# Optimization experiments

Measured on AMD Instinct MI355X. Metric: run time of the kernel, lower is better.

## Reference

```python
import jax, jax.numpy as jnp
import numpy as np

EPSILON = 0.1
NUM_ITERS = 50
D = 256


def setup_inputs() -> dict:
    key = jax.random.key(0)
    ks = jax.random.split(key, 12)
    NA, NT = 8192, 8192
    s = 1.0 / np.sqrt(D)
    return {
        "agent_embeddings": jax.random.normal(ks[0], (NA, D), jnp.float32),
        "task_embeddings": jax.random.normal(ks[1], (NT, D), jnp.float32),
        "Wq": jax.random.normal(ks[2], (D, D), jnp.float32) * s,
        "bq": jax.random.normal(ks[3], (D,), jnp.float32) * 0.01,
        "Wk": jax.random.normal(ks[4], (D, D), jnp.float32) * s,
        "bk": jax.random.normal(ks[5], (D,), jnp.float32) * 0.01,
        "W1": jax.random.normal(ks[6], (D, D // 2), jnp.float32) * s,
        "b1": jax.random.normal(ks[7], (D // 2,), jnp.float32) * 0.01,
        "W2": jax.random.normal(ks[8], (D // 2, 1), jnp.float32) * (1.0 / np.sqrt(D // 2)),
        "b2": jax.random.normal(ks[9], (1,), jnp.float32) * 0.01,
    }


def _ot_forward(agent_embeddings, task_embeddings, Wq, bq, Wk, bk, W1, b1, W2, b2):
    num_tasks = task_embeddings.shape[0]
    q = agent_embeddings @ Wq + bq  # [NA, D]
    k = task_embeddings @ Wk + bk   # [NT, D]
    q_norm = jnp.sum(q * q, axis=1, keepdims=True)          # [NA, 1]
    k_norm = jnp.sum(k * k, axis=1, keepdims=True)          # [NT, 1]
    distances = q_norm + k_norm.T - 2.0 * (q @ k.T)          # [NA, NT]
    C = -distances
    supply_logits = (jax.nn.relu(agent_embeddings @ W1 + b1) @ W2 + b2)[:, 0]
    b = jax.nn.softmax(supply_logits, axis=0)                # [NA]
    a = jnp.ones((num_tasks,), dtype=C.dtype) / num_tasks    # [NT]

    log_b = jnp.log(b + 1e-20)
    log_a = jnp.log(a + 1e-20)
    log_K = -C / EPSILON                                     # [NA, NT]

    def body(_, fg):
        f, g = fg
        f = log_b - jax.nn.logsumexp(log_K + g[None, :], axis=1)
        g = log_a - jax.nn.logsumexp(log_K + f[:, None], axis=0)
        return (f, g)

    f0 = jnp.zeros_like(b)
    g0 = jnp.zeros_like(a)
    f, g = jax.lax.fori_loop(0, NUM_ITERS, body, (f0, g0))

    T = jnp.exp(f[:, None] + log_K + g[None, :])
    T = jnp.maximum(T, 0.0)
    T = T / (jnp.sum(T) + 1e-08)
    return T


def reference(agent_embeddings, task_embeddings, Wq, bq, Wk, bk, W1, b1, W2, b2):
    return _ot_forward(agent_embeddings, task_embeddings, Wq, bq, Wk, bk, W1, b1, W2, b2)
```

## Files before the change

### kernel.cpp

```cpp
#include <hip/hip_runtime.h>
#include <math.h>

#define NR 8192
#define DIM 256
#define NBLK 512
#define CROWS 16
#define RSC 2
#define NSUB 8
#define SCALE2 14.426950408889634f

__device__ __forceinline__ float fexp2(float x) {
#if __has_builtin(__builtin_amdgcn_exp2f)
    return __builtin_amdgcn_exp2f(x);
#else
    return exp2f(x);
#endif
}
__device__ __forceinline__ float flog2(float x) {
#if __has_builtin(__builtin_amdgcn_logf)
    return __builtin_amdgcn_logf(x);
#else
    return log2f(x);
#endif
}

__device__ __forceinline__ void gl2lds16(const float* gp, float* lp) {
#if __has_builtin(__builtin_amdgcn_global_load_lds)
    __builtin_amdgcn_global_load_lds(
        (const __attribute__((address_space(1))) unsigned int*)gp,
        (__attribute__((address_space(3))) unsigned int*)lp, 16, 0, 0);
#else
    *(float4*)lp = *(const float4*)gp;
#endif
}

__device__ __forceinline__ void wait_vm0()  { asm volatile("s_waitcnt vmcnt(0)" ::: "memory"); }
__device__ __forceinline__ void bar_lgkm()  { asm volatile("s_waitcnt lgkmcnt(0)\ns_barrier" ::: "memory"); }

__device__ __forceinline__ void lse_comb2(float& m, float& s, float mo, float so) {
    float nm = fmaxf(m, mo);
    s = s * fexp2(m - nm) + so * fexp2(mo - nm);
    m = nm;
}

__device__ __forceinline__ void lse_upd4(float& m, float& s,
                                         float v0, float v1, float v2, float v3) {
    float m4 = fmaxf(fmaxf(v0, v1), fmaxf(v2, v3));
    float nm = fmaxf(m, m4);
    float e = fexp2(v0 - nm) + fexp2(v1 - nm) + fexp2(v2 - nm) + fexp2(v3 - nm);
    s = fmaf(s, fexp2(m - nm), e);
    m = nm;
}

__device__ __forceinline__ void lse_upd2(float& m, float& s, float v0, float v1) {
    float m2 = fmaxf(v0, v1);
    float nm = fmaxf(m, m2);
    float e = fexp2(v0 - nm) + fexp2(v1 - nm);
    s = fmaf(s, fexp2(m - nm), e);
    m = nm;
}

__global__ void init_zero(float* __restrict__ g) {
    int t = blockIdx.x * 256 + threadIdx.x;
    if (t < NR) g[t] = 0.0f;
}

__global__ __launch_bounds__(256) void gemm_qk(const float* __restrict__ A,
                                               const float* __restrict__ W,
                                               const float* __restrict__ bias,
                                               float* __restrict__ out) {
    __shared__ float As[16][68];
    __shared__ float Ws[16][68];
    const int t  = threadIdx.x;
    const int r0 = blockIdx.x * 64;
    const int c0 = blockIdx.y * 64;
    const int ty = t >> 4, tx = t & 15;
    const int arow = t >> 2;
    const int ak   = (t & 3) * 4;
    const int wrow = t >> 4;
    const int wcol = (t & 15) * 4;
    float acc[4][4] = {};
    for (int k0 = 0; k0 < DIM; k0 += 16) {
        float4 av = *(const float4*)(A + (size_t)(r0 + arow) * DIM + k0 + ak);
        float4 wv = *(const float4*)(W + (size_t)(k0 + wrow) * DIM + c0 + wcol);
        __syncthreads();
        As[ak + 0][arow] = av.x; As[ak + 1][arow] = av.y;
        As[ak + 2][arow] = av.z; As[ak + 3][arow] = av.w;
        *(float4*)&Ws[wrow][wcol] = wv;
        __syncthreads();
#pragma unroll
        for (int kk = 0; kk < 16; ++kk) {
            float4 a = *(const float4*)&As[kk][ty * 4];
            float4 b = *(const float4*)&Ws[kk][tx * 4];
            float aa[4] = {a.x, a.y, a.z, a.w};
            float bb[4] = {b.x, b.y, b.z, b.w};
#pragma unroll
            for (int i = 0; i < 4; ++i)
#pragma unroll
                for (int j = 0; j < 4; ++j)
                    acc[i][j] = fmaf(aa[i], bb[j], acc[i][j]);
        }
    }
#pragma unroll
    for (int i = 0; i < 4; ++i) {
        float4 o;
        o.x = acc[i][0] + bias[c0 + tx * 4 + 0];
        o.y = acc[i][1] + bias[c0 + tx * 4 + 1];
        o.z = acc[i][2] + bias[c0 + tx * 4 + 2];
        o.w = acc[i][3] + bias[c0 + tx * 4 + 3];
        *(float4*)(out + (size_t)(r0 + ty * 4 + i) * DIM + c0 + tx * 4) = o;
    }
}

__global__ __launch_bounds__(64) void row_norm(const float* __restrict__ x,
                                               float* __restrict__ out) {
    const int row = blockIdx.x, lane = threadIdx.x;
    float4 v = *(const float4*)(x + (size_t)row * DIM + lane * 4);
    float s = v.x * v.x + v.y * v.y + v.z * v.z + v.w * v.w;
#pragma unroll
    for (int off = 32; off > 0; off >>= 1) s += __shfl_xor(s, off);
    if (lane == 0) out[row] = s;
}

__global__ __launch_bounds__(128) void mlp_logits(const float* __restrict__ A,
                                                  const float* __restrict__ W1,
                                                  const float* __restrict__ b1,
                                                  const float* __restrict__ W2,
                                                  const float* __restrict__ b2,
                                                  float* __restrict__ logits) {
    __shared__ float ar[DIM];
    __shared__ float red[2];
    const int t = threadIdx.x;
    const int row = blockIdx.x;
    *(float2*)&ar[t * 2] = *(const float2*)(A + (size_t)row * DIM + t * 2);
    __syncthreads();
    float h = b1[t];
#pragma unroll 8
    for (int kk = 0; kk < DIM; ++kk) h = fmaf(ar[kk], W1[kk * 128 + t], h);
    float val = fmaxf(h, 0.0f) * W2[t];
#pragma unroll
    for (int off = 32; off > 0; off >>= 1) val += __shfl_xor(val, off);
    if ((t & 63) == 0) red[t >> 6] = val;
    __syncthreads();
    if (t == 0) logits[row] = red[0] + red[1] + b2[0];
}

__global__ __launch_bounds__(1024) void softmax_logb(const float* __restrict__ logits,
                                                     float* __restrict__ logb2) {
    __shared__ float redm[16], reds[16];
    const int t = threadIdx.x;
    float l[8];
    float m = -INFINITY;
#pragma unroll
    for (int i = 0; i < 8; ++i) { l[i] = logits[i * 1024 + t]; m = fmaxf(m, l[i]); }
#pragma unroll
    for (int off = 32; off > 0; off >>= 1) m = fmaxf(m, __shfl_xor(m, off));
    if ((t & 63) == 0) redm[t >> 6] = m;
    __syncthreads();
    if (t < 64) {
        float v = (t < 16) ? redm[t] : -INFINITY;
#pragma unroll
        for (int off = 8; off > 0; off >>= 1) v = fmaxf(v, __shfl_xor(v, off));
        if (t == 0) redm[0] = v;
    }
    __syncthreads();
    m = redm[0];
    float s = 0.0f;
#pragma unroll
    for (int i = 0; i < 8; ++i) s += __expf(l[i] - m);
#pragma unroll
    for (int off = 32; off > 0; off >>= 1) s += __shfl_xor(s, off);
    if ((t & 63) == 0) reds[t >> 6] = s;
    __syncthreads();
    if (t < 64) {
        float v = (t < 16) ? reds[t] : 0.0f;
#pragma unroll
        for (int off = 8; off > 0; off >>= 1) v += __shfl_xor(v, off);
        if (t == 0) reds[0] = v;
    }
    __syncthreads();
    s = reds[0];
    float invs = 1.0f / s;
#pragma unroll
    for (int i = 0; i < 8; ++i)
        logb2[i * 1024 + t] = log2f(__expf(l[i] - m) * invs + 1e-20f);
}

__global__ __launch_bounds__(256) void dist_kernel(const float* __restrict__ q,
                                                   const float* __restrict__ k,
                                                   const float* __restrict__ qn,
                                                   const float* __restrict__ kn,
                                                   float* __restrict__ S) {
    __shared__ float Qs[16][132];
    __shared__ float Ks[16][132];
    const int t  = threadIdx.x;
    const int r0 = blockIdx.y * 128;
    const int c0 = blockIdx.x * 128;
    const int lrow = t >> 1;
    const int lk   = (t & 1) * 8;
    const int wv   = t >> 6;
    const int lane = t & 63;
    const int ty8 = (wv >> 1) * 8 + (lane >> 3);
    const int tx8 = (wv & 1) * 8 + (lane & 7);
    float acc[8][8] = {};
    for (int k0 = 0; k0 < DIM; k0 += 16) {
        float4 qa = *(const float4*)(q + (size_t)(r0 + lrow) * DIM + k0 + lk);
        float4 qb = *(const float4*)(q + (size_t)(r0 + lrow) * DIM + k0 + lk + 4);
        float4 ka = *(const float4*)(k + (size_t)(c0 + lrow) * DIM + k0 + lk);
        float4 kb = *(const float4*)(k + (size_t)(c0 + lrow) * DIM + k0 + lk + 4);
        __syncthreads();
        Qs[lk + 0][lrow] = qa.x; Qs[lk + 1][lrow] = qa.y;
        Qs[lk + 2][lrow] = qa.z; Qs[lk + 3][lrow] = qa.w;
        Qs[lk + 4][lrow] = qb.x; Qs[lk + 5][lrow] = qb.y;
        Qs[lk + 6][lrow] = qb.z; Qs[lk + 7][lrow] = qb.w;
        Ks[lk + 0][lrow] = ka.x; Ks[lk + 1][lrow] = ka.y;
        Ks[lk + 2][lrow] = ka.z; Ks[lk + 3][lrow] = ka.w;
        Ks[lk + 4][lrow] = kb.x; Ks[lk + 5][lrow] = kb.y;
        Ks[lk + 6][lrow] = kb.z; Ks[lk + 7][lrow] = kb.w;
        __syncthreads();
#pragma unroll
        for (int kk = 0; kk < 16; ++kk) {
            float4 a0 = *(const float4*)&Qs[kk][ty8 * 8];
            float4 a1 = *(const float4*)&Qs[kk][ty8 * 8 + 4];
            float4 b0 = *(const float4*)&Ks[kk][tx8 * 8];
            float4 b1 = *(const float4*)&Ks[kk][tx8 * 8 + 4];
            float aa[8] = {a0.x, a0.y, a0.z, a0.w, a1.x, a1.y, a1.z, a1.w};
            float bb[8] = {b0.x, b0.y, b0.z, b0.w, b1.x, b1.y, b1.z, b1.w};
#pragma unroll
            for (int i = 0; i < 8; ++i)
#pragma unroll
                for (int j = 0; j < 8; ++j)
                    acc[i][j] = fmaf(aa[i], bb[j], acc[i][j]);
        }
    }
    float knv[8];
#pragma unroll
    for (int j = 0; j < 8; ++j) knv[j] = kn[c0 + tx8 * 8 + j];
#pragma unroll
    for (int i = 0; i < 8; ++i) {
        const int row = r0 + ty8 * 8 + i;
        const float qni = qn[row];
        float* outp = S + (size_t)row * NR + c0 + tx8 * 8;
        float4 o0, o1;
        o0.x = (qni + knv[0] - 2.0f * acc[i][0]) * SCALE2;
        o0.y = (qni + knv[1] - 2.0f * acc[i][1]) * SCALE2;
        o0.z = (qni + knv[2] - 2.0f * acc[i][2]) * SCALE2;
        o0.w = (qni + knv[3] - 2.0f * acc[i][3]) * SCALE2;
        o1.x = (qni + knv[4] - 2.0f * acc[i][4]) * SCALE2;
        o1.y = (qni + knv[5] - 2.0f * acc[i][5]) * SCALE2;
        o1.z = (qni + knv[6] - 2.0f * acc[i][6]) * SCALE2;
        o1.w = (qni + knv[7] - 2.0f * acc[i][7]) * SCALE2;
        *(float4*)outp = o0;
        *(float4*)(outp + 4) = o1;
    }
}

__global__ __launch_bounds__(512, 4) void iter_fused(const float* __restrict__ S,
                                                     const float* __restrict__ g,
                                                     const float* __restrict__ logb2,
                                                     float* __restrict__ f,
                                                     float* __restrict__ pm) {
    __shared__ float buf[RSC][NR];
    __shared__ float redm[8], reds[8];
    const int t = threadIdx.x;
    const int wv = t >> 6, lane = t & 63;
    const int chunk = blockIdx.x;
    const int r0 = chunk * CROWS;
    const int rw = wv >> 2;
    const int qt = wv & 3;
    const int qbase = qt * 2048;
    const int loff = lane * 4;

    float4 greg[8];
#pragma unroll
    for (int it = 0; it < 8; ++it)
        greg[it] = *(const float4*)(g + qbase + it * 256 + loff);

    float cm[4][4], cs[4][4];
#pragma unroll
    for (int j = 0; j < 4; ++j)
#pragma unroll
        for (int c = 0; c < 4; ++c) { cm[j][c] = -INFINITY; cs[j][c] = 0.0f; }

    {
        const float* Sr = S + (size_t)(r0 + rw) * NR + qbase;
        float* ld = &buf[rw][qbase];
#pragma unroll
        for (int it = 0; it < 8; ++it)
#if __has_builtin(__builtin_amdgcn_global_load_lds)
            gl2lds16(Sr + it * 256 + loff, ld + it * 256);
#else
            gl2lds16(Sr + it * 256 + loff, ld + it * 256 + loff);
#endif
    }

    for (int sc = 0; sc < NSUB; ++sc) {
        wait_vm0();
        float m = -INFINITY, s = 0.0f;
#pragma unroll
        for (int it = 0; it < 8; ++it) {
            float4 v = *(const float4*)&buf[rw][qbase + it * 256 + loff];
            float4 gv = greg[it];
            lse_upd4(m, s, v.x + gv.x, v.y + gv.y, v.z + gv.z, v.w + gv.w);
        }
#pragma unroll
        for (int off = 32; off > 0; off >>= 1) {
            float mo = __shfl_xor(m, off);
            float so = __shfl_xor(s, off);
            lse_comb2(m, s, mo, so);
        }
        if (lane == 0) { redm[wv] = m; reds[wv] = s; }
        bar_lgkm();

        float fr[RSC];
#pragma unroll
        for (int r = 0; r < RSC; ++r) {
            float mm = redm[r * 4 + 0], ss = reds[r * 4 + 0];
            lse_comb2(mm, ss, redm[r * 4 + 1], reds[r * 4 + 1]);
            lse_comb2(mm, ss, redm[r * 4 + 2], reds[r * 4 + 2]);
            lse_comb2(mm, ss, redm[r * 4 + 3], reds[r * 4 + 3]);
            fr[r] = logb2[r0 + sc * RSC + r] - (mm + flog2(ss));
        }
        if (t < RSC) f[r0 + sc * RSC + t] = fr[t];

#pragma unroll
        for (int j = 0; j < 4; ++j) {
            const int c = j * 2048 + t * 4;
            float4 a = *(const float4*)&buf[0][c];
            float4 bb = *(const float4*)&buf[1][c];
            lse_upd2(cm[j][0], cs[j][0], a.x + fr[0], bb.x + fr[1]);
            lse_upd2(cm[j][1], cs[j][1], a.y + fr[0], bb.y + fr[1]);
            lse_upd2(cm[j][2], cs[j][2], a.z + fr[0], bb.z + fr[1]);
            lse_upd2(cm[j][3], cs[j][3], a.w + fr[0], bb.w + fr[1]);
        }
        bar_lgkm();

        if (sc + 1 < NSUB) {
            const float* Sn = S + (size_t)(r0 + (sc + 1) * RSC + rw) * NR + qbase;
            float* ld = &buf[rw][qbase];
#pragma unroll
            for (int it = 0; it < 8; ++it)
#if __has_builtin(__builtin_amdgcn_global_load_lds)
                gl2lds16(Sn + it * 256 + loff, ld + it * 256);
#else
                gl2lds16(Sn + it * 256 + loff, ld + it * 256 + loff);
#endif
        }
    }
#pragma unroll
    for (int j = 0; j < 4; ++j) {
        float4 L;
        L.x = cm[j][0] + flog2(cs[j][0]);
        L.y = cm[j][1] + flog2(cs[j][1]);
        L.z = cm[j][2] + flog2(cs[j][2]);
        L.w = cm[j][3] + flog2(cs[j][3]);
        *(float4*)&pm[(size_t)chunk * NR + j * 2048 + t * 4] = L;
    }
}

__global__ __launch_bounds__(256) void col_combine(const float* __restrict__ pm,
                                                   float* __restrict__ g,
                                                   float log_a2) {
    __shared__ float Lsh[8][32];
    const int cl = threadIdx.x & 31;
    const int gp = threadIdx.x >> 5;
    const int col = blockIdx.x * 32 + cl;
    float m = -INFINITY, s = 0.0f;
#pragma unroll
    for (int ch = gp * 64; ch < gp * 64 + 64; ch += 4) {
        float l0 = pm[(size_t)(ch + 0) * NR + col];
        float l1 = pm[(size_t)(ch + 1) * NR + col];
        float l2 = pm[(size_t)(ch + 2) * NR + col];
        float l3 = pm[(size_t)(ch + 3) * NR + col];
        lse_upd4(m, s, l0, l1, l2, l3);
    }
    Lsh[gp][cl] = m + flog2(s);
    __syncthreads();
    if (gp == 0) {
        float mm = -INFINITY, ss = 0.0f;
        lse_upd4(mm, ss, Lsh[0][cl], Lsh[1][cl], Lsh[2][cl], Lsh[3][cl]);
        lse_upd4(mm, ss, Lsh[4][cl], Lsh[5][cl], Lsh[6][cl], Lsh[7][cl]);
        g[col] = log_a2 - (mm + flog2(ss));
    }
}

__global__ __launch_bounds__(256) void write_pass(const float* S,
                                                  const float* __restrict__ f,
                                                  const float* __restrict__ g,
                                                  float* out) {
    const int wv = threadIdx.x >> 6, lane = threadIdx.x & 63;
    const int row = blockIdx.x * 4 + wv;
    const float fi = f[row];
    const float4* Sr = (const float4*)(S + (size_t)row * NR);
    const float4* gr = (const float4*)g;
    float4* Or = (float4*)(out + (size_t)row * NR);
#pragma unroll 4
    for (int it = 0; it < NR / 256; ++it) {
        const int idx = it * 64 + lane;
        float4 sv = Sr[idx];
        float4 gv = gr[idx];
        float4 o;
        o.x = fexp2(fi + sv.x + gv.x);
        o.y = fexp2(fi + sv.y + gv.y);
        o.z = fexp2(fi + sv.z + gv.z);
        o.w = fexp2(fi + sv.w + gv.w);
        Or[idx] = o;
    }
}

extern "C" void kernel_launch(void* const* d_in, const int* in_sizes, int n_in,
                              void* d_out, int out_size, void* d_ws, size_t ws_size,
                              hipStream_t stream) {
    (void)in_sizes; (void)n_in; (void)out_size; (void)ws_size;
    const float* A  = (const float*)d_in[0];
    const float* Tk = (const float*)d_in[1];
    const float* Wq = (const float*)d_in[2];
    const float* bq = (const float*)d_in[3];
    const float* Wk = (const float*)d_in[4];
    const float* bk = (const float*)d_in[5];
    const float* W1 = (const float*)d_in[6];
    const float* b1 = (const float*)d_in[7];
    const float* W2 = (const float*)d_in[8];
    const float* b2 = (const float*)d_in[9];
    float* S  = (float*)d_out;
    float* ws = (float*)d_ws;
    float* qn     = ws; ws += NR;
    float* kn     = ws; ws += NR;
    float* logb2  = ws; ws += NR;
    float* logits = ws; ws += NR;
    float* f      = ws; ws += NR;
    float* g      = ws; ws += NR;
    float* pm     = ws; ws += (size_t)NBLK * NR;
    float* q      = ws; ws += (size_t)NR * DIM;
    float* k      = ws; ws += (size_t)NR * DIM;

    const float log_a2 = -13.0f;

    init_zero<<<32, 256, 0, stream>>>(g);
    gemm_qk<<<dim3(128, 4), 256, 0, stream>>>(A, Wq, bq, q);
    gemm_qk<<<dim3(128, 4), 256, 0, stream>>>(Tk, Wk, bk, k);
    row_norm<<<NR, 64, 0, stream>>>(q, qn);
    row_norm<<<NR, 64, 0, stream>>>(k, kn);
    mlp_logits<<<NR, 128, 0, stream>>>(A, W1, b1, W2, b2, logits);
    softmax_logb<<<1, 1024, 0, stream>>>(logits, logb2);
    dist_kernel<<<dim3(64, 64), 256, 0, stream>>>(q, k, qn, kn, S);
    for (int it = 0; it < 50; ++it) {
        iter_fused<<<NBLK, 512, 0, stream>>>(S, g, logb2, f, pm);
        col_combine<<<NR / 32, 256, 0, stream>>>(pm, g, log_a2);
    }
    write_pass<<<NR / 4, 256, 0, stream>>>(S, f, g, S);
}
```

Measured before the change: 3.621 ms.

## Compute distance GEMM with split-bf16 MFMA instead of FP32 FMA

Replaces the FP32 shared-memory tiled distance GEMM with an MFMA bf16 kernel. Each of q and k is split into hi and lo bf16 parts, and four MFMAs per tile recover near-FP32 precision. This targets the FP32 FMA cost of the 8192x8192x256 GEMM. It adds two split kernels and reuses the pm workspace for the bf16 buffers. The new kernel also drops LDS staging, so fragments load straight from global memory and output stores are scalar rather than vectorized.

```diff
diff --git a/kernel.cpp b/kernel.cpp
--- a/kernel.cpp
+++ b/kernel.cpp
@@ -8,6 +8,10 @@
 #define RSC 2
 #define NSUB 8
 #define SCALE2 14.426950408889634f
+
+typedef unsigned short ushort_t;
+typedef __attribute__((ext_vector_type(8))) short bfrag;
+typedef __attribute__((ext_vector_type(4))) float facc;
 
 __device__ __forceinline__ float fexp2(float x) {
 #if __has_builtin(__builtin_amdgcn_exp2f)
@@ -58,6 +62,15 @@
     float e = fexp2(v0 - nm) + fexp2(v1 - nm);
     s = fmaf(s, fexp2(m - nm), e);
     m = nm;
+}
+
+__device__ __forceinline__ ushort_t f2bf(float x) {
+    unsigned u = __float_as_uint(x);
+    u += 0x7FFFu + ((u >> 16) & 1u);
+    return (ushort_t)(u >> 16);
+}
+__device__ __forceinline__ float bf2f(ushort_t b) {
+    return __uint_as_float(((unsigned)b) << 16);
 }
 
 __global__ void init_zero(float* __restrict__ g) {
@@ -122,6 +135,81 @@
     if (lane == 0) out[row] = s;
 }
 
+__global__ __launch_bounds__(256) void split_bf16(const float* __restrict__ x,
+                                                  ushort_t* __restrict__ hi,
+                                                  ushort_t* __restrict__ lo) {
+    const int idx = (blockIdx.x * 256 + threadIdx.x) * 4;
+    float4 v = *(const float4*)(x + idx);
+    ushort_t h0 = f2bf(v.x), h1 = f2bf(v.y), h2 = f2bf(v.z), h3 = f2bf(v.w);
+    ushort4 hv = make_ushort4(h0, h1, h2, h3);
+    ushort4 lv = make_ushort4(f2bf(v.x - bf2f(h0)), f2bf(v.y - bf2f(h1)),
+                              f2bf(v.z - bf2f(h2)), f2bf(v.w - bf2f(h3)));
+    *(ushort4*)(hi + idx) = hv;
+    *(ushort4*)(lo + idx) = lv;
+}
+
+__global__ __launch_bounds__(256) void dist_mfma(const ushort_t* __restrict__ qh,
+                                                 const ushort_t* __restrict__ ql,
+                                                 const ushort_t* __restrict__ kh,
+                                                 const ushort_t* __restrict__ kl,
+                                                 const float* __restrict__ qn,
+                                                 const float* __restrict__ kn,
+                                                 float* __restrict__ S) {
+    const int t = threadIdx.x;
+    const int wv = t >> 6, lane = t & 63;
+    const int r0 = blockIdx.y * 128 + (wv >> 1) * 64;
+    const int c0 = blockIdx.x * 128 + (wv & 1) * 64;
+    const int fr = lane & 15;
+    const int fq = lane >> 4;
+    facc acc[4][4];
+#pragma unroll
+    for (int i = 0; i < 4; ++i)
+#pragma unroll
+        for (int j = 0; j < 4; ++j) acc[i][j] = (facc){0.f, 0.f, 0.f, 0.f};
+
+    for (int k0 = 0; k0 < DIM; k0 += 32) {
+        const int ks = k0 + fq * 8;
+        bfrag ah[4], al[4], bh[4], bl[4];
+#pragma unroll
+        for (int mi = 0; mi < 4; ++mi) {
+            const size_t ao = (size_t)(r0 + mi * 16 + fr) * DIM + ks;
+            ah[mi] = *(const bfrag*)(qh + ao);
+            al[mi] = *(const bfrag*)(ql + ao);
+        }
+#pragma unroll
+        for (int ni = 0; ni < 4; ++ni) {
+            const size_t bo = (size_t)(c0 + ni * 16 + fr) * DIM + ks;
+            bh[ni] = *(const bfrag*)(kh + bo);
+            bl[ni] = *(const bfrag*)(kl + bo);
+        }
+#pragma unroll
+        for (int mi = 0; mi < 4; ++mi)
+#pragma unroll
+            for (int ni = 0; ni < 4; ++ni) {
+                acc[mi][ni] = __builtin_amdgcn_mfma_f32_16x16x32_bf16(ah[mi], bh[ni], acc[mi][ni], 0, 0, 0);
+                acc[mi][ni] = __builtin_amdgcn_mfma_f32_16x16x32_bf16(ah[mi], bl[ni], acc[mi][ni], 0, 0, 0);
+                acc[mi][ni] = __builtin_amdgcn_mfma_f32_16x16x32_bf16(al[mi], bh[ni], acc[mi][ni], 0, 0, 0);
+                acc[mi][ni] = __builtin_amdgcn_mfma_f32_16x16x32_bf16(al[mi], bl[ni], acc[mi][ni], 0, 0, 0);
+            }
+    }
+#pragma unroll
+    for (int mi = 0; mi < 4; ++mi) {
+        float qnr[4];
+#pragma unroll
+        for (int r = 0; r < 4; ++r) qnr[r] = qn[r0 + mi * 16 + fq * 4 + r];
+#pragma unroll
+        for (int ni = 0; ni < 4; ++ni) {
+            const int col = c0 + ni * 16 + fr;
+            const float knc = kn[col];
+#pragma unroll
+            for (int r = 0; r < 4; ++r) {
+                const int row = r0 + mi * 16 + fq * 4 + r;
+                S[(size_t)row * NR + col] = (qnr[r] + knc - 2.0f * acc[mi][ni][r]) * SCALE2;
+            }
+        }
+    }
+}
+
 __global__ __launch_bounds__(128) void mlp_logits(const float* __restrict__ A,
                                                   const float* __restrict__ W1,
                                                   const float* __restrict__ b1,
@@ -184,75 +272,6 @@
 #pragma unroll
     for (int i = 0; i < 8; ++i)
         logb2[i * 1024 + t] = log2f(__expf(l[i] - m) * invs + 1e-20f);
-}
-
-__global__ __launch_bounds__(256) void dist_kernel(const float* __restrict__ q,
-                                                   const float* __restrict__ k,
-                                                   const float* __restrict__ qn,
-                                                   const float* __restrict__ kn,
-                                                   float* __restrict__ S) {
-    __shared__ float Qs[16][132];
-    __shared__ float Ks[16][132];
-    const int t  = threadIdx.x;
-    const int r0 = blockIdx.y * 128;
-    const int c0 = blockIdx.x * 128;
-    const int lrow = t >> 1;
-    const int lk   = (t & 1) * 8;
-    const int wv   = t >> 6;
-    const int lane = t & 63;
-    const int ty8 = (wv >> 1) * 8 + (lane >> 3);
-    const int tx8 = (wv & 1) * 8 + (lane & 7);
-    float acc[8][8] = {};
-    for (int k0 = 0; k0 < DIM; k0 += 16) {
-        float4 qa = *(const float4*)(q + (size_t)(r0 + lrow) * DIM + k0 + lk);
-        float4 qb = *(const float4*)(q + (size_t)(r0 + lrow) * DIM + k0 + lk + 4);
-        float4 ka = *(const float4*)(k + (size_t)(c0 + lrow) * DIM + k0 + lk);
-        float4 kb = *(const float4*)(k + (size_t)(c0 + lrow) * DIM + k0 + lk + 4);
-        __syncthreads();
-        Qs[lk + 0][lrow] = qa.x; Qs[lk + 1][lrow] = qa.y;
-        Qs[lk + 2][lrow] = qa.z; Qs[lk + 3][lrow] = qa.w;
-        Qs[lk + 4][lrow] = qb.x; Qs[lk + 5][lrow] = qb.y;
-        Qs[lk + 6][lrow] = qb.z; Qs[lk + 7][lrow] = qb.w;
-        Ks[lk + 0][lrow] = ka.x; Ks[lk + 1][lrow] = ka.y;
-        Ks[lk + 2][lrow] = ka.z; Ks[lk + 3][lrow] = ka.w;
-        Ks[lk + 4][lrow] = kb.x; Ks[lk + 5][lrow] = kb.y;
-        Ks[lk + 6][lrow] = kb.z; Ks[lk + 7][lrow] = kb.w;
-        __syncthreads();
-#pragma unroll
-        for (int kk = 0; kk < 16; ++kk) {
-            float4 a0 = *(const float4*)&Qs[kk][ty8 * 8];
-            float4 a1 = *(const float4*)&Qs[kk][ty8 * 8 + 4];
-            float4 b0 = *(const float4*)&Ks[kk][tx8 * 8];
-            float4 b1 = *(const float4*)&Ks[kk][tx8 * 8 + 4];
-            float aa[8] = {a0.x, a0.y, a0.z, a0.w, a1.x, a1.y, a1.z, a1.w};
-            float bb[8] = {b0.x, b0.y, b0.z, b0.w, b1.x, b1.y, b1.z, b1.w};
-#pragma unroll
-            for (int i = 0; i < 8; ++i)
-#pragma unroll
-                for (int j = 0; j < 8; ++j)
-                    acc[i][j] = fmaf(aa[i], bb[j], acc[i][j]);
-        }
-    }
-    float knv[8];
-#pragma unroll
-    for (int j = 0; j < 8; ++j) knv[j] = kn[c0 + tx8 * 8 + j];
-#pragma unroll
-    for (int i = 0; i < 8; ++i) {
-        const int row = r0 + ty8 * 8 + i;
-        const float qni = qn[row];
-        float* outp = S + (size_t)row * NR + c0 + tx8 * 8;
-        float4 o0, o1;
-        o0.x = (qni + knv[0] - 2.0f * acc[i][0]) * SCALE2;
-        o0.y = (qni + knv[1] - 2.0f * acc[i][1]) * SCALE2;
-        o0.z = (qni + knv[2] - 2.0f * acc[i][2]) * SCALE2;
-        o0.w = (qni + knv[3] - 2.0f * acc[i][3]) * SCALE2;
-        o1.x = (qni + knv[4] - 2.0f * acc[i][4]) * SCALE2;
-        o1.y = (qni + knv[5] - 2.0f * acc[i][5]) * SCALE2;
-        o1.z = (qni + knv[6] - 2.0f * acc[i][6]) * SCALE2;
-        o1.w = (qni + knv[7] - 2.0f * acc[i][7]) * SCALE2;
-        *(float4*)outp = o0;
-        *(float4*)(outp + 4) = o1;
-    }
 }
 
 __global__ __launch_bounds__(512, 4) void iter_fused(const float* __restrict__ S,
@@ -433,6 +452,10 @@
     float* pm     = ws; ws += (size_t)NBLK * NR;
     float* q      = ws; ws += (size_t)NR * DIM;
     float* k      = ws; ws += (size_t)NR * DIM;
+    ushort_t* qh = (ushort_t*)pm;
+    ushort_t* ql = qh + (size_t)NR * DIM;
+    ushort_t* kh = ql + (size_t)NR * DIM;
+    ushort_t* kl = kh + (size_t)NR * DIM;
 
     const float log_a2 = -13.0f;
 
@@ -441,9 +464,11 @@
     gemm_qk<<<dim3(128, 4), 256, 0, stream>>>(Tk, Wk, bk, k);
     row_norm<<<NR, 64, 0, stream>>>(q, qn);
     row_norm<<<NR, 64, 0, stream>>>(k, kn);
+    split_bf16<<<NR * DIM / 1024, 256, 0, stream>>>(q, qh, ql);
+    split_bf16<<<NR * DIM / 1024, 256, 0, stream>>>(k, kh, kl);
     mlp_logits<<<NR, 128, 0, stream>>>(A, W1, b1, W2, b2, logits);
     softmax_logb<<<1, 1024, 0, stream>>>(logits, logb2);
-    dist_kernel<<<dim3(64, 64), 256, 0, stream>>>(q, k, qn, kn, S);
+    dist_mfma<<<dim3(64, 64), 256, 0, stream>>>(qh, ql, kh, kl, qn, kn, S);
     for (int it = 0; it < 50; ++it) {
         iter_fused<<<NBLK, 512, 0, stream>>>(S, g, logb2, f, pm);
         col_combine<<<NR / 32, 256, 0, stream>>>(pm, g, log_a2);
```

Measured after the change: 3.438 ms. 5.1% less time.
